# Kernel optimization log

Measured on AMD Instinct MI355X. Metric: run time of the kernel, lower is better.

## Reference

```python
import jax, jax.numpy as jnp
import numpy as np

B, L, H, C = 1, 512, 1024, 2


def setup_inputs() -> dict:
    key = jax.random.key(0)
    k1, k2, k3 = jax.random.split(key, 3)
    lm_output = jax.random.normal(k1, (B, L, H), dtype=jnp.float32)
    # torch Linear weight layout: [out_features, in_features]
    W1 = jax.random.normal(k2, (H, 2 * H), dtype=jnp.float32) * 0.02
    b1 = jnp.zeros((H,), dtype=jnp.float32)
    W2 = jax.random.normal(k3, (C, H), dtype=jnp.float32) * 0.02
    b2 = jnp.zeros((C,), dtype=jnp.float32)
    return {"lm_output": lm_output, "W1": W1, "b1": b1, "W2": W2, "b2": b2}


def reference(lm_output, W1, b1, W2, b2):
    # pair_emb[b,i,j] = concat(lm_output[b,j], lm_output[b,i])
    # Linear(concat(a,b)) decomposes: split W1 into the halves acting on each part.
    Wa = W1[:, :H]  # acts on lm_output_a (the j / column token)
    Wb = W1[:, H:]  # acts on lm_output_b (the i / row token)
    a_proj = jnp.einsum('blh,oh->blo', lm_output, Wa)  # [B,L,H]
    b_proj = jnp.einsum('blh,oh->blo', lm_output, Wb)  # [B,L,H]
    # hidden[b,i,j] = tanh(a_proj[b,j] + b_proj[b,i] + b1)   -> [B,L,L,H]
    hidden = jnp.tanh(a_proj[:, None, :, :] + b_proj[:, :, None, :] + b1)
    # Dropout is identity at inference time.
    logits = jnp.einsum('bijh,ch->bijc', hidden, W2) + b2  # [B,L,L,C]
    logits = (logits + jnp.swapaxes(logits, 1, 2)) / 2.0
    return logits
```

## Files before the change

### kernel.cpp

```cpp
#include <hip/hip_runtime.h>
#include <hip/hip_bf16.h>

#define HH 1024
#define LL 512
#define TNT 8
#define NTILE 36

typedef __attribute__((ext_vector_type(8))) short bf16x8;
typedef __attribute__((ext_vector_type(4))) float f32x4;
typedef __attribute__((ext_vector_type(2))) float f32x2;

static constexpr float C_EXP = 2.8853900817779268f;

static __device__ __forceinline__ uint4 pack8(float4 a, float4 b) {
    union { uint4 u; __hip_bfloat162 h[4]; } r;
    r.h[0] = __float22bfloat162_rn(make_float2(a.x, a.y));
    r.h[1] = __float22bfloat162_rn(make_float2(a.z, a.w));
    r.h[2] = __float22bfloat162_rn(make_float2(b.x, b.y));
    r.h[3] = __float22bfloat162_rn(make_float2(b.z, b.w));
    return r.u;
}

static __device__ __forceinline__ f32x2 lo2(const float4& v) { return (f32x2){v.x, v.y}; }
static __device__ __forceinline__ f32x2 hi2(const float4& v) { return (f32x2){v.z, v.w}; }

__global__ __launch_bounds__(256, 4) void proj_mfma_kernel(
    const float* __restrict__ lm, const float* __restrict__ W1,
    const float* __restrict__ b1, float* __restrict__ Ea, float* __restrict__ Eb)
{
    __shared__ ushort As[64][136];
    __shared__ ushort Bs[64][136];

    const int tid  = threadIdx.x;
    const int lane = tid & 63;
    const int w    = tid >> 6;
    const int b    = blockIdx.x;
    const int xcd  = b & 7;
    const int idx  = b >> 3;
    const int nbase = (xcd * 4 + (idx & 3)) * 64;
    const int mbase = (idx >> 2) * 64;
    const int wm   = w * 16;
    const int sel  = nbase >> 10;
    const int nrow = nbase & 1023;

    const int frow = lane & 15;
    const int q8   = (lane >> 4) * 8;

    f32x4 acc[4] = {};

    for (int kb = 0; kb < HH; kb += 128) {
        __syncthreads();
        {
            int p = tid;
#pragma unroll
            for (int it = 0; it < 4; ++it, p += 256) {
                const int row = p >> 4, c8 = (p & 15) * 8;
                const float* pa = &lm[(mbase + row) * HH + kb + c8];
                *(uint4*)&As[row][c8] = pack8(*(const float4*)pa, *(const float4*)(pa + 4));
                const float* pw = &W1[(nrow + row) * 2048 + sel * 1024 + kb + c8];
                *(uint4*)&Bs[row][c8] = pack8(*(const float4*)pw, *(const float4*)(pw + 4));
            }
        }
        __syncthreads();

#pragma unroll
        for (int s = 0; s < 4; ++s) {
            const bf16x8 a = *(const bf16x8*)&As[wm + frow][s * 32 + q8];
#pragma unroll
            for (int nf = 0; nf < 4; ++nf) {
                const bf16x8 bb = *(const bf16x8*)&Bs[nf * 16 + frow][s * 32 + q8];
                acc[nf] = __builtin_amdgcn_mfma_f32_16x16x32_bf16(a, bb, acc[nf], 0, 0, 0);
            }
        }
    }

    const int col = lane & 15;
    const int rq  = (lane >> 4) * 4;
    const int m0  = mbase + wm + rq;
    const bool isA = sel == 0;
#pragma unroll
    for (int nf = 0; nf < 4; ++nf) {
        const int nn = (nrow + nf * 16 + col);
        if (isA) {
            const float bb = b1[nn];
#pragma unroll
            for (int r = 0; r < 4; ++r)
                Ea[(m0 + r) * HH + nn] = __builtin_amdgcn_exp2f(C_EXP * (acc[nf][r] + bb));
        } else {
#pragma unroll
            for (int r = 0; r < 4; ++r)
                Eb[(m0 + r) * HH + nn] = __builtin_amdgcn_exp2f(C_EXP * acc[nf][r]);
        }
    }
}

__global__ __launch_bounds__(256, 3) void pair_kernel(
    const float* __restrict__ Ea, const float* __restrict__ Eb,
    const float* __restrict__ W2, float* __restrict__ pbuf, int slice)
{
    __shared__ float tl[4][64][32];

    const int tid = threadIdx.x;
    const int tx  = tid & 15;
    const int ty  = tid >> 4;

    int tt = blockIdx.x, bi = 0, rem = TNT;
    while (tt >= rem) { tt -= rem; --rem; ++bi; }
    const int bj    = bi + tt;
    const int ibase = bi * 64;
    const int jbase = bj * 64;
    const int k0    = blockIdx.y * slice;

    f32x2 acc0[4][4] = {};
    f32x2 acc1[4][4] = {};
    const f32x2 one2 = {1.f, 1.f};

    for (int kb = 0; kb < slice; kb += 32) {
        if (kb) __syncthreads();
        {
            const int c4  = tid & 7;
            const int r0  = tid >> 3;
            const int hof = k0 + kb + c4 * 4;
#pragma unroll
            for (int it = 0; it < 8; ++it) {
                const int tile = it >> 1;
                const int row  = (it & 1) * 32 + r0;
                const int base = (tile < 2) ? jbase : ibase;
                const float* src = (tile == 0 || tile == 2) ? Ea : Eb;
                const int c4s = c4 ^ (row & 7);
                *(float4*)&tl[tile][row][c4s * 4] =
                    *(const float4*)&src[(size_t)(base + row) * HH + hof];
            }
        }
        __syncthreads();

#pragma unroll 2
        for (int h4 = 0; h4 < 8; ++h4) {
            const int sxj = (h4 ^ (tx & 7)) * 4;
            const int sxi = (h4 ^ (ty & 7)) * 4;
            float4 Aj[4], Bj[4], Ai[4], Bi[4];
#pragma unroll
            for (int jj = 0; jj < 4; ++jj) {
                Aj[jj] = *(const float4*)&tl[0][tx + 16 * jj][sxj];
                Bj[jj] = *(const float4*)&tl[1][tx + 16 * jj][sxj];
            }
#pragma unroll
            for (int ii = 0; ii < 4; ++ii) {
                Ai[ii] = *(const float4*)&tl[2][ty + 16 * ii][sxi];
                Bi[ii] = *(const float4*)&tl[3][ty + 16 * ii][sxi];
            }
            const float4 w0q = *(const float4*)&W2[k0 + kb + h4 * 4];
            const float4 w1q = *(const float4*)&W2[HH + k0 + kb + h4 * 4];
            const f32x2 w0lo = lo2(w0q), w0hi = hi2(w0q);
            const f32x2 w1lo = lo2(w1q), w1hi = hi2(w1q);

#pragma unroll
            for (int ii = 0; ii < 4; ++ii) {
                const f32x2 ailo = lo2(Ai[ii]), aihi = hi2(Ai[ii]);
                const f32x2 bilo = lo2(Bi[ii]), bihi = hi2(Bi[ii]);
#pragma unroll
                for (int jj = 0; jj < 4; ++jj) {
                    const f32x2 d01 = __builtin_elementwise_fma(bilo, lo2(Aj[jj]), one2);
                    const f32x2 d23 = __builtin_elementwise_fma(bihi, hi2(Aj[jj]), one2);
                    const f32x2 e01 = __builtin_elementwise_fma(ailo, lo2(Bj[jj]), one2);
                    const f32x2 e23 = __builtin_elementwise_fma(aihi, hi2(Bj[jj]), one2);
                    const f32x2 n01 = d01 + e01, n23 = d23 + e23;
                    const f32x2 m01 = d01 * e01, m23 = d23 * e23;
                    const float p01 = m01.x * m01.y;
                    const float p23 = m23.x * m23.y;
                    const float R   = __builtin_amdgcn_rcpf(p01 * p23);
                    const float r01 = R * p23;
                    const float r23 = R * p01;
                    const f32x2 u01 = (n01 * __builtin_shufflevector(m01, m01, 1, 0))
                                      * (f32x2){r01, r01};
                    const f32x2 u23 = (n23 * __builtin_shufflevector(m23, m23, 1, 0))
                                      * (f32x2){r23, r23};
                    acc0[ii][jj] = __builtin_elementwise_fma(u01, w0lo, acc0[ii][jj]);
                    acc0[ii][jj] = __builtin_elementwise_fma(u23, w0hi, acc0[ii][jj]);
                    acc1[ii][jj] = __builtin_elementwise_fma(u01, w1lo, acc1[ii][jj]);
                    acc1[ii][jj] = __builtin_elementwise_fma(u23, w1hi, acc1[ii][jj]);
                }
            }
        }
    }

    float* pb = pbuf + ((size_t)blockIdx.y * NTILE + blockIdx.x) * 8192;
#pragma unroll
    for (int ii = 0; ii < 4; ++ii)
#pragma unroll
        for (int jj = 0; jj < 4; ++jj) {
            const int li = ty + 16 * ii, lj = tx + 16 * jj;
            const f32x2 v = { acc0[ii][jj].x + acc0[ii][jj].y,
                              acc1[ii][jj].x + acc1[ii][jj].y };
            *(f32x2*)&pb[(li * 64 + lj) * 2] = v;
        }
}

__global__ __launch_bounds__(256) void combine_kernel(
    const float* __restrict__ pbuf, const float* __restrict__ W2,
    const float* __restrict__ b2, float* __restrict__ out, int nz)
{
    __shared__ float s_ws[2];

    const int tid = threadIdx.x;
    if (tid < 128) {
        const int c = tid >> 6, l = tid & 63;
        float s = 0.f;
#pragma unroll
        for (int q = 0; q < 4; ++q) {
            const float4 v = *(const float4*)&W2[c * HH + (l + q * 64) * 4];
            s += v.x + v.y + v.z + v.w;
        }
#pragma unroll
        for (int off = 32; off; off >>= 1) s += __shfl_down(s, off, 64);
        if (l == 0) s_ws[c] = s + b2[c];
    }
    __syncthreads();

    const int idx   = blockIdx.x * 256 + tid;
    const int t     = idx >> 13;
    const int local = idx & 8191;
    int tt = t, bi = 0, rem = TNT;
    while (tt >= rem) { tt -= rem; --rem; ++bi; }
    const int bj = bi + tt;

    float s0 = 0.f, s1 = 0.f, s2 = 0.f, s3 = 0.f;
    for (int z = 0; z < nz; z += 4) {
        s0 += pbuf[((size_t)z * NTILE + t) * 8192 + local];
        s1 += pbuf[((size_t)(z + 1) * NTILE + t) * 8192 + local];
        s2 += pbuf[((size_t)(z + 2) * NTILE + t) * 8192 + local];
        s3 += pbuf[((size_t)(z + 3) * NTILE + t) * 8192 + local];
    }
    const float s = (s0 + s1) + (s2 + s3);

    const int li = local >> 7;
    const int lj = (local >> 1) & 63;
    const int c  = local & 1;
    const float v = s_ws[c] - s;

    const int i = bi * 64 + li;
    const int j = bj * 64 + lj;
    out[(i * LL + j) * 2 + c] = v;
    out[(j * LL + i) * 2 + c] = v;
}

extern "C" void kernel_launch(void* const* d_in, const int* in_sizes, int n_in,
                              void* d_out, int out_size, void* d_ws, size_t ws_size,
                              hipStream_t stream)
{
    const float* lm = (const float*)d_in[0];
    const float* W1 = (const float*)d_in[1];
    const float* b1 = (const float*)d_in[2];
    const float* W2 = (const float*)d_in[3];
    const float* b2 = (const float*)d_in[4];
    float* out = (float*)d_out;

    char* ws = (char*)d_ws;
    float* Ea   = (float*)ws;
    float* Eb   = (float*)(ws + (2u << 20));
    float* pbuf = (float*)(ws + (4u << 20) + 64);

    const size_t ubase = (4u << 20) + 64;
    const size_t per_z = (size_t)NTILE * 8192 * 4;
    int nz = 8;
    if      (ws_size >= ubase + 32 * per_z) nz = 32;
    else if (ws_size >= ubase + 16 * per_z) nz = 16;
    const int slice = HH / nz;

    proj_mfma_kernel<<<256, 256, 0, stream>>>(lm, W1, b1, Ea, Eb);
    pair_kernel<<<dim3(NTILE, nz), 256, 0, stream>>>(Ea, Eb, W2, pbuf, slice);
    combine_kernel<<<(NTILE * 8192) / 256, 256, 0, stream>>>(pbuf, W2, b2, out, nz);
}
```

Before: 129.2 us.

## Halve proj N-tile to double grid; restructure pair inner loop to stream j loads

The projection GEMM now uses 64x32 tiles instead of 64x64 and launches 512 blocks instead of 256, to fill more compute units on the first stage. In the pair kernel the inner loop is reordered: i-side values are preloaded as f32x2 halves, j-side tiles are loaded one at a time inside the jj loop, and the h4 loop is no longer unrolled. Together these aim to lower register pressure. Vector types switch from float4 to ext_vector f32x4 so the halves are taken with shufflevector. The smaller projection tile re-reads the lm tile more often, and with no unrolling there is less room to hide LDS latency.

```diff
diff --git a/kernel.cpp b/kernel.cpp
--- a/kernel.cpp
+++ b/kernel.cpp
@@ -12,7 +12,7 @@
 
 static constexpr float C_EXP = 2.8853900817779268f;
 
-static __device__ __forceinline__ uint4 pack8(float4 a, float4 b) {
+static __device__ __forceinline__ uint4 pack8(f32x4 a, f32x4 b) {
     union { uint4 u; __hip_bfloat162 h[4]; } r;
     r.h[0] = __float22bfloat162_rn(make_float2(a.x, a.y));
     r.h[1] = __float22bfloat162_rn(make_float2(a.z, a.w));
@@ -21,15 +21,15 @@
     return r.u;
 }
 
-static __device__ __forceinline__ f32x2 lo2(const float4& v) { return (f32x2){v.x, v.y}; }
-static __device__ __forceinline__ f32x2 hi2(const float4& v) { return (f32x2){v.z, v.w}; }
+static __device__ __forceinline__ f32x2 lo2(f32x4 v) { return __builtin_shufflevector(v, v, 0, 1); }
+static __device__ __forceinline__ f32x2 hi2(f32x4 v) { return __builtin_shufflevector(v, v, 2, 3); }
 
 __global__ __launch_bounds__(256, 4) void proj_mfma_kernel(
     const float* __restrict__ lm, const float* __restrict__ W1,
     const float* __restrict__ b1, float* __restrict__ Ea, float* __restrict__ Eb)
 {
     __shared__ ushort As[64][136];
-    __shared__ ushort Bs[64][136];
+    __shared__ ushort Bs[32][136];
 
     const int tid  = threadIdx.x;
     const int lane = tid & 63;
@@ -37,8 +37,8 @@
     const int b    = blockIdx.x;
     const int xcd  = b & 7;
     const int idx  = b >> 3;
-    const int nbase = (xcd * 4 + (idx & 3)) * 64;
-    const int mbase = (idx >> 2) * 64;
+    const int nbase = (xcd * 8 + (idx & 7)) * 32;
+    const int mbase = (idx >> 3) * 64;
     const int wm   = w * 16;
     const int sel  = nbase >> 10;
     const int nrow = nbase & 1023;
@@ -46,7 +46,7 @@
     const int frow = lane & 15;
     const int q8   = (lane >> 4) * 8;
 
-    f32x4 acc[4] = {};
+    f32x4 acc[2] = {};
 
     for (int kb = 0; kb < HH; kb += 128) {
         __syncthreads();
@@ -56,9 +56,14 @@
             for (int it = 0; it < 4; ++it, p += 256) {
                 const int row = p >> 4, c8 = (p & 15) * 8;
                 const float* pa = &lm[(mbase + row) * HH + kb + c8];
-                *(uint4*)&As[row][c8] = pack8(*(const float4*)pa, *(const float4*)(pa + 4));
+                *(uint4*)&As[row][c8] = pack8(*(const f32x4*)pa, *(const f32x4*)(pa + 4));
+            }
+            int q = tid;
+#pragma unroll
+            for (int it = 0; it < 2; ++it, q += 256) {
+                const int row = q >> 4, c8 = (q & 15) * 8;
                 const float* pw = &W1[(nrow + row) * 2048 + sel * 1024 + kb + c8];
-                *(uint4*)&Bs[row][c8] = pack8(*(const float4*)pw, *(const float4*)(pw + 4));
+                *(uint4*)&Bs[row][c8] = pack8(*(const f32x4*)pw, *(const f32x4*)(pw + 4));
             }
         }
         __syncthreads();
@@ -67,7 +72,7 @@
         for (int s = 0; s < 4; ++s) {
             const bf16x8 a = *(const bf16x8*)&As[wm + frow][s * 32 + q8];
 #pragma unroll
-            for (int nf = 0; nf < 4; ++nf) {
+            for (int nf = 0; nf < 2; ++nf) {
                 const bf16x8 bb = *(const bf16x8*)&Bs[nf * 16 + frow][s * 32 + q8];
                 acc[nf] = __builtin_amdgcn_mfma_f32_16x16x32_bf16(a, bb, acc[nf], 0, 0, 0);
             }
@@ -79,7 +84,7 @@
     const int m0  = mbase + wm + rq;
     const bool isA = sel == 0;
 #pragma unroll
-    for (int nf = 0; nf < 4; ++nf) {
+    for (int nf = 0; nf < 2; ++nf) {
         const int nn = (nrow + nf * 16 + col);
         if (isA) {
             const float bb = b1[nn];
@@ -128,42 +133,42 @@
                 const int base = (tile < 2) ? jbase : ibase;
                 const float* src = (tile == 0 || tile == 2) ? Ea : Eb;
                 const int c4s = c4 ^ (row & 7);
-                *(float4*)&tl[tile][row][c4s * 4] =
-                    *(const float4*)&src[(size_t)(base + row) * HH + hof];
+                *(f32x4*)&tl[tile][row][c4s * 4] =
+                    *(const f32x4*)&src[(size_t)(base + row) * HH + hof];
             }
         }
         __syncthreads();
 
-#pragma unroll 2
+#pragma unroll 1
         for (int h4 = 0; h4 < 8; ++h4) {
             const int sxj = (h4 ^ (tx & 7)) * 4;
             const int sxi = (h4 ^ (ty & 7)) * 4;
-            float4 Aj[4], Bj[4], Ai[4], Bi[4];
-#pragma unroll
-            for (int jj = 0; jj < 4; ++jj) {
-                Aj[jj] = *(const float4*)&tl[0][tx + 16 * jj][sxj];
-                Bj[jj] = *(const float4*)&tl[1][tx + 16 * jj][sxj];
-            }
+
+            f32x2 ailo[4], aihi[4], bilo[4], bihi[4];
 #pragma unroll
             for (int ii = 0; ii < 4; ++ii) {
-                Ai[ii] = *(const float4*)&tl[2][ty + 16 * ii][sxi];
-                Bi[ii] = *(const float4*)&tl[3][ty + 16 * ii][sxi];
-            }
-            const float4 w0q = *(const float4*)&W2[k0 + kb + h4 * 4];
-            const float4 w1q = *(const float4*)&W2[HH + k0 + kb + h4 * 4];
+                const f32x4 Ai = *(const f32x4*)&tl[2][ty + 16 * ii][sxi];
+                const f32x4 Bi = *(const f32x4*)&tl[3][ty + 16 * ii][sxi];
+                ailo[ii] = lo2(Ai); aihi[ii] = hi2(Ai);
+                bilo[ii] = lo2(Bi); bihi[ii] = hi2(Bi);
+            }
+            const f32x4 w0q = *(const f32x4*)&W2[k0 + kb + h4 * 4];
+            const f32x4 w1q = *(const f32x4*)&W2[HH + k0 + kb + h4 * 4];
             const f32x2 w0lo = lo2(w0q), w0hi = hi2(w0q);
             const f32x2 w1lo = lo2(w1q), w1hi = hi2(w1q);
 
 #pragma unroll
-            for (int ii = 0; ii < 4; ++ii) {
-                const f32x2 ailo = lo2(Ai[ii]), aihi = hi2(Ai[ii]);
-                const f32x2 bilo = lo2(Bi[ii]), bihi = hi2(Bi[ii]);
-#pragma unroll
-                for (int jj = 0; jj < 4; ++jj) {
-                    const f32x2 d01 = __builtin_elementwise_fma(bilo, lo2(Aj[jj]), one2);
-                    const f32x2 d23 = __builtin_elementwise_fma(bihi, hi2(Aj[jj]), one2);
-                    const f32x2 e01 = __builtin_elementwise_fma(ailo, lo2(Bj[jj]), one2);
-                    const f32x2 e23 = __builtin_elementwise_fma(aihi, hi2(Bj[jj]), one2);
+            for (int jj = 0; jj < 4; ++jj) {
+                const f32x4 Aj = *(const f32x4*)&tl[0][tx + 16 * jj][sxj];
+                const f32x4 Bj = *(const f32x4*)&tl[1][tx + 16 * jj][sxj];
+                const f32x2 ajlo = lo2(Aj), ajhi = hi2(Aj);
+                const f32x2 bjlo = lo2(Bj), bjhi = hi2(Bj);
+#pragma unroll
+                for (int ii = 0; ii < 4; ++ii) {
+                    const f32x2 d01 = __builtin_elementwise_fma(bilo[ii], ajlo, one2);
+                    const f32x2 d23 = __builtin_elementwise_fma(bihi[ii], ajhi, one2);
+                    const f32x2 e01 = __builtin_elementwise_fma(ailo[ii], bjlo, one2);
+                    const f32x2 e23 = __builtin_elementwise_fma(aihi[ii], bjhi, one2);
                     const f32x2 n01 = d01 + e01, n23 = d23 + e23;
                     const f32x2 m01 = d01 * e01, m23 = d23 * e23;
                     const float p01 = m01.x * m01.y;
@@ -208,7 +213,7 @@
         float s = 0.f;
 #pragma unroll
         for (int q = 0; q < 4; ++q) {
-            const float4 v = *(const float4*)&W2[c * HH + (l + q * 64) * 4];
+            const f32x4 v = *(const f32x4*)&W2[c * HH + (l + q * 64) * 4];
             s += v.x + v.y + v.z + v.w;
         }
 #pragma unroll
@@ -267,7 +272,7 @@
     else if (ws_size >= ubase + 16 * per_z) nz = 16;
     const int slice = HH / nz;
 
-    proj_mfma_kernel<<<256, 256, 0, stream>>>(lm, W1, b1, Ea, Eb);
+    proj_mfma_kernel<<<512, 256, 0, stream>>>(lm, W1, b1, Ea, Eb);
     pair_kernel<<<dim3(NTILE, nz), 256, 0, stream>>>(Ea, Eb, W2, pbuf, slice);
     combine_kernel<<<(NTILE * 8192) / 256, 256, 0, stream>>>(pbuf, W2, b2, out, nz);
 }
```

New measurement: 129.0 us. No clear change (-0.2%).
